# Kernel tuning notes

Measured on AMD Instinct MI355X. Metric: run time of the kernel, lower is better.

The kernel has to match this reference:

```python
import jax, jax.numpy as jnp
import numpy as np

H = 8  # num_heads (init kwarg)

def setup_inputs() -> dict:
    key = jax.random.key(0)
    k1, k2, k3, k4 = jax.random.split(key, 4)
    B, S, E = 4, 2048, 512
    x = jax.random.normal(k1, (B, S, E), dtype=jnp.float32)
    # 'normal' keras initializer ~ N(0, 0.05)
    Wq = jax.random.normal(k2, (E, E), dtype=jnp.float32) * 0.05
    Wk = jax.random.normal(k3, (E, E), dtype=jnp.float32) * 0.05
    Wv = jax.random.normal(k4, (E, E), dtype=jnp.float32) * 0.05
    return {"x": x, "Wq": Wq, "Wk": Wk, "Wv": Wv}

def _split_heads(t):
    # [B,S,E] -> [H,B,S,E/H]; matches tf.stack(tf.split(t, H, axis=2))
    B, S, E = t.shape
    return t.reshape(B, S, H, E // H).transpose(2, 0, 1, 3)

def reference(x, Wq, Wk, Wv):
    B, S, E = x.shape
    q = _split_heads(jnp.einsum('bse,ef->bsf', x, Wq))  # [H,B,S,dh]
    k = _split_heads(jnp.einsum('bse,ef->bsf', x, Wk))
    v = _split_heads(jnp.einsum('bse,ef->bsf', x, Wv))
    # NOTE: original has NO 1/sqrt(d) scaling
    scores = jnp.einsum('hbqd,hbkd->hbqk', q, k)         # [H,B,S,S]
    attn = jax.nn.softmax(scores, axis=-1)
    effect = jnp.einsum('hbqk,hbkd->hbqd', attn, v)      # [H,B,S,dh]
    # tf.concat(tf.split(effect, H), axis=-1) + squeeze == merge heads on last dim
    out = effect.transpose(1, 2, 0, 3).reshape(B, S, E)  # [B,S,E]
    return (out, x)
```

## Files before the change

### kernel.cpp

```cpp
#include <hip/hip_runtime.h>

typedef _Float16 f16x8 __attribute__((ext_vector_type(8)));
typedef __fp16 h16x2 __attribute__((ext_vector_type(2)));
typedef float f32x4 __attribute__((ext_vector_type(4)));
typedef float f32x16 __attribute__((ext_vector_type(16)));

#define GF(r) ((((r)&3)) ^ (((r)>>2)&3))
#define LOG2E 1.44269504088896f

#define GLD16(gp, lp) __builtin_amdgcn_global_load_lds( \
    (const __attribute__((address_space(1))) void*)(gp), \
    (__attribute__((address_space(3))) void*)(lp), 16, 0, 0)

__global__ void cvt_x_kernel(const float4* __restrict__ x4, f16x8* __restrict__ xh,
                             float4* __restrict__ xc, int n8) {
    int i = blockIdx.x * 256 + threadIdx.x;
    if (i >= n8) return;
    float4 a = x4[2 * i], b = x4[2 * i + 1];
    xc[2 * i] = a;
    xc[2 * i + 1] = b;
    f16x8 h;
    h[0] = (_Float16)a.x; h[1] = (_Float16)a.y; h[2] = (_Float16)a.z; h[3] = (_Float16)a.w;
    h[4] = (_Float16)b.x; h[5] = (_Float16)b.y; h[6] = (_Float16)b.z; h[7] = (_Float16)b.w;
    xh[i] = h;
}

__global__ void cvt_w_kernel(const float* __restrict__ Wq, const float* __restrict__ Wk,
                             const float* __restrict__ Wv, _Float16* __restrict__ wt) {
    int j = blockIdx.x * 256 + threadIdx.x;
    if (j >= 786432) return;
    int mat = j >> 18;
    int r = (j >> 9) & 511;
    int n = j & 511;
    const float* W = (mat == 0) ? Wq : ((mat == 1) ? Wk : Wv);
    float v = W[r * 512 + n];
    wt[(size_t)mat * 262144 + (size_t)n * 512 + r] = (_Float16)v;
}

__global__ __launch_bounds__(256, 2) void gemm_qkv(
    const _Float16* __restrict__ xh, const _Float16* __restrict__ wt,
    _Float16* __restrict__ qh, _Float16* __restrict__ kh, _Float16* __restrict__ vt) {
    __shared__ __align__(16) char gsm[49152];
    const int mat = blockIdx.y;
    const _Float16* wp = wt + (size_t)mat * 262144;
    const int mtile = blockIdx.x >> 2, ntile = blockIdx.x & 3;
    const int tid = threadIdx.x, lane = tid & 63;
    const int g = lane >> 4, c = lane & 15;
    const int wid = tid >> 6, wm = wid >> 1, wn = wid & 1;

    f32x4 acc[4][4];
#pragma unroll
    for (int i = 0; i < 4; ++i)
#pragma unroll
        for (int j = 0; j < 4; ++j) acc[i][j] = (f32x4){0.f, 0.f, 0.f, 0.f};

    const int row0 = tid >> 2, p0 = tid & 3;

    auto GSTAGE = [&](int buf, int ks) {
        _Float16* la_ = (_Float16*)(gsm + buf * 16384);
        _Float16* lb_ = (_Float16*)(gsm + buf * 16384 + 8192);
        int r = row0, pp = p0 ^ GF(r);
        GLD16(xh + (size_t)(mtile * 128 + r) * 512 + ks * 32 + pp * 8, &la_[tid * 8]);
        GLD16(wp + (size_t)(ntile * 128 + r) * 512 + ks * 32 + pp * 8, &lb_[tid * 8]);
        r = 64 + row0; pp = p0 ^ GF(r);
        GLD16(xh + (size_t)(mtile * 128 + r) * 512 + ks * 32 + pp * 8, &la_[(256 + tid) * 8]);
        GLD16(wp + (size_t)(ntile * 128 + r) * 512 + ks * 32 + pp * 8, &lb_[(256 + tid) * 8]);
    };

    auto GTILE = [&](int ks) {
        const _Float16* la = (const _Float16*)(gsm + (ks % 3) * 16384);
        const _Float16* lb = (const _Float16*)(gsm + (ks % 3) * 16384 + 8192);
        f16x8 af[4], bf[4];
#pragma unroll
        for (int i = 0; i < 4; ++i) {
            int ra = wm * 64 + i * 16 + c;
            af[i] = *(const f16x8*)&la[ra * 32 + ((g ^ GF(ra)) * 8)];
            int rb = wn * 64 + i * 16 + c;
            bf[i] = *(const f16x8*)&lb[rb * 32 + ((g ^ GF(rb)) * 8)];
        }
        __builtin_amdgcn_s_setprio(1);
#pragma unroll
        for (int mi = 0; mi < 4; ++mi)
#pragma unroll
            for (int ni = 0; ni < 4; ++ni)
                acc[mi][ni] = __builtin_amdgcn_mfma_f32_16x16x32_f16(af[mi], bf[ni], acc[mi][ni], 0, 0, 0);
        __builtin_amdgcn_s_setprio(0);
    };

    GSTAGE(0, 0); GSTAGE(1, 1);
#pragma unroll 1
    for (int ks = 0; ks < 14; ++ks) {
        asm volatile("s_waitcnt vmcnt(4)" ::: "memory");
        __builtin_amdgcn_s_barrier();
        __builtin_amdgcn_sched_barrier(0);
        GSTAGE((ks + 2) % 3, ks + 2);
        GTILE(ks);
    }
    asm volatile("s_waitcnt vmcnt(4)" ::: "memory");
    __builtin_amdgcn_s_barrier();
    GTILE(14);
    asm volatile("s_waitcnt vmcnt(0)" ::: "memory");
    __builtin_amdgcn_s_barrier();
    GTILE(15);

#pragma unroll
    for (int mi = 0; mi < 4; ++mi)
#pragma unroll
        for (int ni = 0; ni < 4; ++ni)
#pragma unroll
            for (int r = 0; r < 4; ++r) {
                int m = mtile * 128 + wm * 64 + mi * 16 + g * 4 + r;
                int n = ntile * 128 + wn * 64 + ni * 16 + c;
                _Float16 hv = (_Float16)acc[mi][ni][r];
                if (mat == 0) {
                    qh[(size_t)m * 512 + n] = hv;
                } else if (mat == 1) {
                    kh[(size_t)m * 512 + n] = hv;
                } else {
                    int h = n >> 6, d = n & 63, bb = m >> 11, s = m & 2047;
                    vt[(((size_t)h * 4 + bb) * 64 + d) * 2048 + s] = hv;
                }
            }
}

__global__ __launch_bounds__(512, 4) void attn_kernel(
    const _Float16* __restrict__ qh, const _Float16* __restrict__ kh,
    const _Float16* __restrict__ vt, float* __restrict__ out) {
    __shared__ __align__(16) char smem[65536];

    const int bid = blockIdx.x;
    const int xcd = bid & 7, idx = bid >> 3;
    const int hb = xcd * 4 + (idx >> 4);
    const int qblk = idx & 15;
    const int h = hb >> 2, b = hb & 3;
    const int tid = threadIdx.x, lane = tid & 63, wid = tid >> 6;
    const int qg = wid & 3, half = wid >> 2;
    const int q = lane & 31, hi = lane >> 5;

    const int qrow0 = qblk * 128 + qg * 32;
    const _Float16* qp = qh + ((size_t)b * 2048 + qrow0) * 512 + h * 64;
    const _Float16* kp = kh + (size_t)b * 2048 * 512 + h * 64;
    const _Float16* vp = vt + (size_t)hb * 64 * 2048;

    const int srow = tid >> 3;
    const int ssw = (tid & 7) ^ (srow & 7);

    auto STAGE = [&](int i) {
        char* base = smem + (i & 1) * 32768;
        GLD16(kp + ((size_t)(i * 64 + srow) * 512) + ssw * 8, (_Float16*)(base) + tid * 8);
        GLD16(vp + (size_t)srow * 2048 + i * 64 + ssw * 8, (_Float16*)(base + 8192) + tid * 8);
        GLD16(kp + ((size_t)((16 + i) * 64 + srow) * 512) + ssw * 8, (_Float16*)(base + 16384) + tid * 8);
        GLD16(vp + (size_t)srow * 2048 + (16 + i) * 64 + ssw * 8, (_Float16*)(base + 24576) + tid * 8);
    };

    f16x8 aQ[4];
#pragma unroll
    for (int kc = 0; kc < 4; ++kc)
        aQ[kc] = *(const f16x8*)(qp + (size_t)q * 512 + kc * 16 + hi * 8);

    float mrow = -1e30f, lrow = 0.f;
    f32x16 o0, o1;
#pragma unroll
    for (int i = 0; i < 16; ++i) { o0[i] = 0.f; o1[i] = 0.f; }

    const h16x2 ONE2 = {(__fp16)1.0f, (__fp16)1.0f};

    auto TILE = [&](int it) {
        const _Float16* kb = (const _Float16*)(smem + (it & 1) * 32768 + half * 16384);
        const _Float16* vb = kb + 4096;

        f32x16 s0, s1;
        __builtin_amdgcn_s_setprio(1);
        {
            f32x16 z0, z1;
#pragma unroll
            for (int i = 0; i < 16; ++i) { z0[i] = 0.f; z1[i] = 0.f; }
            const int r0 = q, r1 = 32 + q, sw = q & 7;
#pragma unroll
            for (int kc = 0; kc < 4; ++kc) {
                f16x8 ak0 = *(const f16x8*)&kb[r0 * 64 + (((2 * kc + hi) ^ sw) * 8)];
                f16x8 ak1 = *(const f16x8*)&kb[r1 * 64 + (((2 * kc + hi) ^ sw) * 8)];
                z0 = __builtin_amdgcn_mfma_f32_32x32x16_f16(ak0, aQ[kc], z0, 0, 0, 0);
                z1 = __builtin_amdgcn_mfma_f32_32x32x16_f16(ak1, aQ[kc], z1, 0, 0, 0);
            }
            s0 = z0; s1 = z1;
        }
        __builtin_amdgcn_s_setprio(0);

        float pm;
        {
            float m0 = fmaxf(fmaxf(fmaxf(s0[0], s0[1]), s0[2]), s0[3]);
            float m1 = fmaxf(fmaxf(fmaxf(s0[4], s0[5]), s0[6]), s0[7]);
            float m2 = fmaxf(fmaxf(fmaxf(s0[8], s0[9]), s0[10]), s0[11]);
            float m3 = fmaxf(fmaxf(fmaxf(s0[12], s0[13]), s0[14]), s0[15]);
            float m4 = fmaxf(fmaxf(fmaxf(s1[0], s1[1]), s1[2]), s1[3]);
            float m5 = fmaxf(fmaxf(fmaxf(s1[4], s1[5]), s1[6]), s1[7]);
            float m6 = fmaxf(fmaxf(fmaxf(s1[8], s1[9]), s1[10]), s1[11]);
            float m7 = fmaxf(fmaxf(fmaxf(s1[12], s1[13]), s1[14]), s1[15]);
            float t0 = fmaxf(fmaxf(m0, m1), m2);
            float t1 = fmaxf(fmaxf(m3, m4), m5);
            float t2 = fmaxf(m6, m7);
            pm = fmaxf(fmaxf(t0, t1), t2);
        }
        pm = fmaxf(pm, __shfl_xor(pm, 32));
        if (__any(pm > mrow + 8.0f)) {
            const float nm = fmaxf(mrow, pm);
            const float e = __builtin_amdgcn_exp2f((mrow - nm) * LOG2E);
            mrow = nm;
            lrow *= e;
            o0 *= e;
            o1 *= e;
        }
        const float nm2 = mrow * LOG2E;

#pragma unroll
        for (int i = 0; i < 16; ++i)
            s0[i] = __builtin_amdgcn_exp2f(fmaf(s0[i], LOG2E, -nm2));
#pragma unroll
        for (int i = 0; i < 16; ++i)
            s1[i] = __builtin_amdgcn_exp2f(fmaf(s1[i], LOG2E, -nm2));

        f16x8 pf[4];
        float rs = 0.f;
#pragma unroll
        for (int kb2 = 0; kb2 < 2; ++kb2) {
            const f32x16& sv = kb2 ? s1 : s0;
            h16x2 p0 = __builtin_amdgcn_cvt_pkrtz(sv[0], sv[1]);
            h16x2 p1 = __builtin_amdgcn_cvt_pkrtz(sv[2], sv[3]);
            h16x2 p2 = __builtin_amdgcn_cvt_pkrtz(sv[4], sv[5]);
            h16x2 p3 = __builtin_amdgcn_cvt_pkrtz(sv[6], sv[7]);
            h16x2 p4 = __builtin_amdgcn_cvt_pkrtz(sv[8], sv[9]);
            h16x2 p5 = __builtin_amdgcn_cvt_pkrtz(sv[10], sv[11]);
            h16x2 p6 = __builtin_amdgcn_cvt_pkrtz(sv[12], sv[13]);
            h16x2 p7 = __builtin_amdgcn_cvt_pkrtz(sv[14], sv[15]);
            rs = __builtin_amdgcn_fdot2(p0, ONE2, rs, false);
            rs = __builtin_amdgcn_fdot2(p1, ONE2, rs, false);
            rs = __builtin_amdgcn_fdot2(p2, ONE2, rs, false);
            rs = __builtin_amdgcn_fdot2(p3, ONE2, rs, false);
            rs = __builtin_amdgcn_fdot2(p4, ONE2, rs, false);
            rs = __builtin_amdgcn_fdot2(p5, ONE2, rs, false);
            rs = __builtin_amdgcn_fdot2(p6, ONE2, rs, false);
            rs = __builtin_amdgcn_fdot2(p7, ONE2, rs, false);
            unsigned t0 = __builtin_bit_cast(unsigned, p0);
            unsigned t1 = __builtin_bit_cast(unsigned, p1);
            unsigned t2 = __builtin_bit_cast(unsigned, p2);
            unsigned t3 = __builtin_bit_cast(unsigned, p3);
            unsigned t4 = __builtin_bit_cast(unsigned, p4);
            unsigned t5 = __builtin_bit_cast(unsigned, p5);
            unsigned t6 = __builtin_bit_cast(unsigned, p6);
            unsigned t7 = __builtin_bit_cast(unsigned, p7);
            asm volatile("v_permlane32_swap_b32 %0, %1" : "+v"(t0), "+v"(t2));
            asm volatile("v_permlane32_swap_b32 %0, %1" : "+v"(t1), "+v"(t3));
            asm volatile("v_permlane32_swap_b32 %0, %1" : "+v"(t4), "+v"(t6));
            asm volatile("v_permlane32_swap_b32 %0, %1" : "+v"(t5), "+v"(t7));
            uint4 u0; u0.x = t0; u0.y = t1; u0.z = t2; u0.w = t3;
            uint4 u1; u1.x = t4; u1.y = t5; u1.z = t6; u1.w = t7;
            pf[2 * kb2 + 0] = __builtin_bit_cast(f16x8, u0);
            pf[2 * kb2 + 1] = __builtin_bit_cast(f16x8, u1);
        }
        lrow += rs;

        __builtin_amdgcn_s_setprio(1);
        {
            const int d0 = q, d1 = 32 + q, sw = q & 7;
#pragma unroll
            for (int ck = 0; ck < 4; ++ck) {
                f16x8 av0 = *(const f16x8*)&vb[d0 * 64 + (((2 * ck + hi) ^ sw) * 8)];
                f16x8 av1 = *(const f16x8*)&vb[d1 * 64 + (((2 * ck + hi) ^ sw) * 8)];
                o0 = __builtin_amdgcn_mfma_f32_32x32x16_f16(av0, pf[ck], o0, 0, 0, 0);
                o1 = __builtin_amdgcn_mfma_f32_32x32x16_f16(av1, pf[ck], o1, 0, 0, 0);
            }
        }
        __builtin_amdgcn_s_setprio(0);
    };

    STAGE(0);
#pragma unroll 1
    for (int it = 0; it < 16; ++it) {
        asm volatile("s_waitcnt vmcnt(0)" ::: "memory");
        __builtin_amdgcn_s_barrier();
        __builtin_amdgcn_sched_barrier(0);
        if (it < 15) STAGE(it + 1);
        TILE(it);
    }

    lrow += __shfl_xor(lrow, 32);
    __builtin_amdgcn_s_barrier();

    float* xg = (float*)smem + qg * 2112;
    if (half) {
#pragma unroll
        for (int i = 0; i < 16; ++i) {
            xg[i * 64 + lane] = o0[i];
            xg[(16 + i) * 64 + lane] = o1[i];
        }
        if (!hi) { xg[2048 + q] = mrow; xg[2080 + q] = lrow; }
    }
    __syncthreads();
    if (!half) {
        const float m_b = xg[2048 + q], l_b = xg[2080 + q];
        const float m = fmaxf(mrow, m_b);
        const float e_a = __builtin_amdgcn_exp2f((mrow - m) * LOG2E);
        const float e_b = __builtin_amdgcn_exp2f((m_b - m) * LOG2E);
        const float inv = 1.0f / (lrow * e_a + l_b * e_b);
        const float sa = e_a * inv, sb = e_b * inv;
#pragma unroll
        for (int i = 0; i < 16; ++i) {
            o0[i] = o0[i] * sa + xg[i * 64 + lane] * sb;
            o1[i] = o1[i] * sa + xg[(16 + i) * 64 + lane] * sb;
        }
        asm volatile("s_waitcnt lgkmcnt(0)" ::: "memory");
#pragma unroll
        for (int i = 0; i < 16; ++i) {
            int dr = (i & 3) + 8 * (i >> 2) + 4 * hi;
            xg[dr * 33 + q] = o0[i];
            xg[(32 + dr) * 33 + q] = o1[i];
        }
        __builtin_amdgcn_s_waitcnt(0);
        const int d0c = (lane & 15) * 4;
#pragma unroll
        for (int i2 = 0; i2 < 8; ++i2) {
            int qr = 4 * i2 + (lane >> 4);
            float4 v;
            v.x = xg[(d0c + 0) * 33 + qr];
            v.y = xg[(d0c + 1) * 33 + qr];
            v.z = xg[(d0c + 2) * 33 + qr];
            v.w = xg[(d0c + 3) * 33 + qr];
            *(float4*)(out + ((size_t)b * 2048 + qrow0 + qr) * 512 + h * 64 + d0c) = v;
        }
    }
}

extern "C" void kernel_launch(void* const* d_in, const int* in_sizes, int n_in,
                              void* d_out, int out_size, void* d_ws, size_t ws_size,
                              hipStream_t stream) {
    const float* x = (const float*)d_in[0];
    const float* Wq = (const float*)d_in[1];
    const float* Wk = (const float*)d_in[2];
    const float* Wv = (const float*)d_in[3];
    float* out = (float*)d_out;
    float* xcopy = out + 4194304;

    char* ws = (char*)d_ws;
    _Float16* xh = (_Float16*)ws;
    _Float16* wt = (_Float16*)(ws + (size_t)(10u << 20));
    _Float16* qh = (_Float16*)(ws + (size_t)(12u << 20));
    _Float16* kh = (_Float16*)(ws + (size_t)(20u << 20));
    _Float16* vt = (_Float16*)(ws + (size_t)(28u << 20));

    cvt_x_kernel<<<2048, 256, 0, stream>>>((const float4*)x, (f16x8*)xh, (float4*)xcopy, 524288);
    cvt_w_kernel<<<3072, 256, 0, stream>>>(Wq, Wk, Wv, wt);
    gemm_qkv<<<dim3(256, 3), 256, 0, stream>>>(xh, wt, qh, kh, vt);
    attn_kernel<<<512, 512, 0, stream>>>(qh, kh, vt, out);
}
```

Before: 93.54 us.

## Merge conversion kernels, refine LDS swizzle, split row-sum accumulator chain

```diff
diff --git a/kernel.cpp b/kernel.cpp
--- a/kernel.cpp
+++ b/kernel.cpp
@@ -12,29 +12,29 @@
     (const __attribute__((address_space(1))) void*)(gp), \
     (__attribute__((address_space(3))) void*)(lp), 16, 0, 0)
 
-__global__ void cvt_x_kernel(const float4* __restrict__ x4, f16x8* __restrict__ xh,
-                             float4* __restrict__ xc, int n8) {
-    int i = blockIdx.x * 256 + threadIdx.x;
-    if (i >= n8) return;
-    float4 a = x4[2 * i], b = x4[2 * i + 1];
-    xc[2 * i] = a;
-    xc[2 * i + 1] = b;
-    f16x8 h;
-    h[0] = (_Float16)a.x; h[1] = (_Float16)a.y; h[2] = (_Float16)a.z; h[3] = (_Float16)a.w;
-    h[4] = (_Float16)b.x; h[5] = (_Float16)b.y; h[6] = (_Float16)b.z; h[7] = (_Float16)b.w;
-    xh[i] = h;
-}
-
-__global__ void cvt_w_kernel(const float* __restrict__ Wq, const float* __restrict__ Wk,
-                             const float* __restrict__ Wv, _Float16* __restrict__ wt) {
-    int j = blockIdx.x * 256 + threadIdx.x;
-    if (j >= 786432) return;
-    int mat = j >> 18;
-    int r = (j >> 9) & 511;
-    int n = j & 511;
-    const float* W = (mat == 0) ? Wq : ((mat == 1) ? Wk : Wv);
-    float v = W[r * 512 + n];
-    wt[(size_t)mat * 262144 + (size_t)n * 512 + r] = (_Float16)v;
+__global__ void cvt_all_kernel(const float4* __restrict__ x4, f16x8* __restrict__ xh,
+                               float4* __restrict__ xc,
+                               const float* __restrict__ Wq, const float* __restrict__ Wk,
+                               const float* __restrict__ Wv, _Float16* __restrict__ wt) {
+    const int blk = blockIdx.x;
+    if (blk < 2048) {
+        int i = blk * 256 + threadIdx.x;
+        float4 a = x4[2 * i], b = x4[2 * i + 1];
+        xc[2 * i] = a;
+        xc[2 * i + 1] = b;
+        f16x8 h;
+        h[0] = (_Float16)a.x; h[1] = (_Float16)a.y; h[2] = (_Float16)a.z; h[3] = (_Float16)a.w;
+        h[4] = (_Float16)b.x; h[5] = (_Float16)b.y; h[6] = (_Float16)b.z; h[7] = (_Float16)b.w;
+        xh[i] = h;
+    } else {
+        int j = (blk - 2048) * 256 + threadIdx.x;
+        int mat = j >> 18;
+        int r = (j >> 9) & 511;
+        int n = j & 511;
+        const float* W = (mat == 0) ? Wq : ((mat == 1) ? Wk : Wv);
+        float v = W[r * 512 + n];
+        wt[(size_t)mat * 262144 + (size_t)n * 512 + r] = (_Float16)v;
+    }
 }
 
 __global__ __launch_bounds__(256, 2) void gemm_qkv(
@@ -143,7 +143,7 @@
     const _Float16* vp = vt + (size_t)hb * 64 * 2048;
 
     const int srow = tid >> 3;
-    const int ssw = (tid & 7) ^ (srow & 7);
+    const int ssw = (tid & 7) ^ ((srow ^ (srow >> 3)) & 7);
 
     auto STAGE = [&](int i) {
         char* base = smem + (i & 1) * 32768;
@@ -164,6 +164,8 @@
     for (int i = 0; i < 16; ++i) { o0[i] = 0.f; o1[i] = 0.f; }
 
     const h16x2 ONE2 = {(__fp16)1.0f, (__fp16)1.0f};
+    const int swr0 = (q ^ (q >> 3)) & 7;
+    const int swr1 = ((32 + q) ^ ((32 + q) >> 3)) & 7;
 
     auto TILE = [&](int it) {
         const _Float16* kb = (const _Float16*)(smem + (it & 1) * 32768 + half * 16384);
@@ -175,11 +177,10 @@
             f32x16 z0, z1;
 #pragma unroll
             for (int i = 0; i < 16; ++i) { z0[i] = 0.f; z1[i] = 0.f; }
-            const int r0 = q, r1 = 32 + q, sw = q & 7;
 #pragma unroll
             for (int kc = 0; kc < 4; ++kc) {
-                f16x8 ak0 = *(const f16x8*)&kb[r0 * 64 + (((2 * kc + hi) ^ sw) * 8)];
-                f16x8 ak1 = *(const f16x8*)&kb[r1 * 64 + (((2 * kc + hi) ^ sw) * 8)];
+                f16x8 ak0 = *(const f16x8*)&kb[q * 64 + (((2 * kc + hi) ^ swr0) * 8)];
+                f16x8 ak1 = *(const f16x8*)&kb[(32 + q) * 64 + (((2 * kc + hi) ^ swr1) * 8)];
                 z0 = __builtin_amdgcn_mfma_f32_32x32x16_f16(ak0, aQ[kc], z0, 0, 0, 0);
                 z1 = __builtin_amdgcn_mfma_f32_32x32x16_f16(ak1, aQ[kc], z1, 0, 0, 0);
             }
@@ -221,7 +222,7 @@
             s1[i] = __builtin_amdgcn_exp2f(fmaf(s1[i], LOG2E, -nm2));
 
         f16x8 pf[4];
-        float rs = 0.f;
+        float rsA = 0.f, rsB = 0.f;
 #pragma unroll
         for (int kb2 = 0; kb2 < 2; ++kb2) {
             const f32x16& sv = kb2 ? s1 : s0;
@@ -233,14 +234,14 @@
             h16x2 p5 = __builtin_amdgcn_cvt_pkrtz(sv[10], sv[11]);
             h16x2 p6 = __builtin_amdgcn_cvt_pkrtz(sv[12], sv[13]);
             h16x2 p7 = __builtin_amdgcn_cvt_pkrtz(sv[14], sv[15]);
-            rs = __builtin_amdgcn_fdot2(p0, ONE2, rs, false);
-            rs = __builtin_amdgcn_fdot2(p1, ONE2, rs, false);
-            rs = __builtin_amdgcn_fdot2(p2, ONE2, rs, false);
-            rs = __builtin_amdgcn_fdot2(p3, ONE2, rs, false);
-            rs = __builtin_amdgcn_fdot2(p4, ONE2, rs, false);
-            rs = __builtin_amdgcn_fdot2(p5, ONE2, rs, false);
-            rs = __builtin_amdgcn_fdot2(p6, ONE2, rs, false);
-            rs = __builtin_amdgcn_fdot2(p7, ONE2, rs, false);
+            rsA = __builtin_amdgcn_fdot2(p0, ONE2, rsA, false);
+            rsB = __builtin_amdgcn_fdot2(p1, ONE2, rsB, false);
+            rsA = __builtin_amdgcn_fdot2(p2, ONE2, rsA, false);
+            rsB = __builtin_amdgcn_fdot2(p3, ONE2, rsB, false);
+            rsA = __builtin_amdgcn_fdot2(p4, ONE2, rsA, false);
+            rsB = __builtin_amdgcn_fdot2(p5, ONE2, rsB, false);
+            rsA = __builtin_amdgcn_fdot2(p6, ONE2, rsA, false);
+            rsB = __builtin_amdgcn_fdot2(p7, ONE2, rsB, false);
             unsigned t0 = __builtin_bit_cast(unsigned, p0);
             unsigned t1 = __builtin_bit_cast(unsigned, p1);
             unsigned t2 = __builtin_bit_cast(unsigned, p2);
@@ -258,15 +259,14 @@
             pf[2 * kb2 + 0] = __builtin_bit_cast(f16x8, u0);
             pf[2 * kb2 + 1] = __builtin_bit_cast(f16x8, u1);
         }
-        lrow += rs;
+        lrow += rsA + rsB;
 
         __builtin_amdgcn_s_setprio(1);
         {
-            const int d0 = q, d1 = 32 + q, sw = q & 7;
 #pragma unroll
             for (int ck = 0; ck < 4; ++ck) {
-                f16x8 av0 = *(const f16x8*)&vb[d0 * 64 + (((2 * ck + hi) ^ sw) * 8)];
-                f16x8 av1 = *(const f16x8*)&vb[d1 * 64 + (((2 * ck + hi) ^ sw) * 8)];
+                f16x8 av0 = *(const f16x8*)&vb[q * 64 + (((2 * ck + hi) ^ swr0) * 8)];
+                f16x8 av1 = *(const f16x8*)&vb[(32 + q) * 64 + (((2 * ck + hi) ^ swr1) * 8)];
                 o0 = __builtin_amdgcn_mfma_f32_32x32x16_f16(av0, pf[ck], o0, 0, 0, 0);
                 o1 = __builtin_amdgcn_mfma_f32_32x32x16_f16(av1, pf[ck], o1, 0, 0, 0);
             }
@@ -348,8 +348,8 @@
     _Float16* kh = (_Float16*)(ws + (size_t)(20u << 20));
     _Float16* vt = (_Float16*)(ws + (size_t)(28u << 20));
 
-    cvt_x_kernel<<<2048, 256, 0, stream>>>((const float4*)x, (f16x8*)xh, (float4*)xcopy, 524288);
-    cvt_w_kernel<<<3072, 256, 0, stream>>>(Wq, Wk, Wv, wt);
+    cvt_all_kernel<<<5120, 256, 0, stream>>>((const float4*)x, (f16x8*)xh, (float4*)xcopy,
+                                             Wq, Wk, Wv, wt);
     gemm_qkv<<<dim3(256, 3), 256, 0, stream>>>(xh, wt, qh, kh, vt);
     attn_kernel<<<512, 512, 0, stream>>>(qh, kh, vt, out);
 }
```

Result: faster. 90.87 us (-2.8%).
